# Kernel tuning notes

Measured on AMD Instinct MI355X. Metric: run time of the kernel, lower is better.

## Reference

```python
import jax, jax.numpy as jnp
import numpy as np


def setup_inputs() -> dict:
    key = jax.random.key(0)
    k1, k2 = jax.random.split(key)
    pred = jax.random.normal(k1, (128, 1024), dtype=jnp.float32)
    y = jax.random.normal(k2, (128, 1024), dtype=jnp.float32)
    return {"pred": pred, "y": y}


def reference(pred, y):
    # Original: transpose to [N, C], then per-column soft Kendall tau.
    p = pred.T  # [N, C]
    l = y.T     # [N, C]
    n = p.shape[0]
    # Pairwise outer differences, batched across all C columns at once: [N, N, C]
    diff = p[:, None, :] - p[None, :, :]
    sgn = jnp.sign(l[:, None, :] - l[None, :, :])
    tmp = jnp.tanh(diff * sgn)
    # Diagonal entries are tanh(0) = 0, so subtracting the eye-masked diagonal
    # (as in the original) is a no-op; just sum everything.
    per_col = jnp.sum(tmp, axis=(0, 1)) / (n * (n - 1))  # [C]
    return 1.0 - per_col.mean()
```

## Files before the change

### kernel.cpp

```cpp
#include <hip/hip_runtime.h>


typedef float v2f __attribute__((ext_vector_type(2)));

#define TAU_N 1024
#define TAU_C 128
#define TILE  256
#define NTILE (TAU_N / TILE)
#define NTP   (NTILE * (NTILE + 1) / 2)
#define PBLK  256
#define THR   1024
#define JOBS  ((TAU_C * NTP) / PBLK)
#define IT    4
#define JSL   16
#define JT    (TILE / JSL)

__device__ __constant__ int c_TI[NTP] = {0,1,1,2,2,2,3,3,3,3};
__device__ __constant__ int c_TJ[NTP] = {0,0,1,0,1,2,0,1,2,3};

__global__ __launch_bounds__(THR) void tau_tri_kernel(
        const float* __restrict__ pred, const float* __restrict__ y,
        float* __restrict__ out, float* __restrict__ acc_ws,
        unsigned* __restrict__ cnt_ws) {
    __shared__ __align__(16) float2 col[TAU_N];
    __shared__ float wsum[THR / 64];

    const int bx   = blockIdx.x;
    const int tid  = threadIdx.x;
    const int lane = tid & 63;
    const int wv   = tid >> 6;

    const int c = bx >> 1;
    const float* p = pred + c * TAU_N;
    const float* l = y    + c * TAU_N;

    col[tid] = make_float2(tanhf(p[tid]), l[tid]);
    __syncthreads();

    const float4* col4 = (const float4*)col;
    const v2f one2 = {1.f, 1.f};
    float acc_tot = 0.f;

#pragma unroll
    for (int q = 0; q < JOBS; ++q) {
        const int job = (bx & 1) * JOBS + q;
        const int ti  = c_TI[job];
        const int tj  = c_TJ[job];

        float mt[IT], ml[IT];
#pragma unroll
        for (int k = 0; k < IT; ++k) {
            float2 v = col[ti * TILE + lane * IT + k];
            mt[k] = v.x; ml[k] = v.y;
        }

        const int jb = (tj * TILE + wv * JT) >> 1;
        v2f acc[IT] = {{0.f,0.f},{0.f,0.f},{0.f,0.f},{0.f,0.f}};
#pragma unroll
        for (int jj = 0; jj < JT / 2; ++jj) {
            float4 qv = col4[jb + jj];
            v2f t2 = {qv.x, qv.z};
            v2f l2 = {qv.y, qv.w};
#pragma unroll
            for (int k = 0; k < IT; ++k) {
                v2f mt2 = {mt[k], mt[k]};
                v2f n2  = mt2 - t2;
                v2f d2  = __builtin_elementwise_fma(-mt2, t2, one2);
                v2f r2  = {__builtin_amdgcn_rcpf(d2.x),
                           __builtin_amdgcn_rcpf(d2.y)};
                v2f v2  = n2 * r2;
                v2f ld2 = (v2f){ml[k], ml[k]} - l2;
                unsigned sx = __float_as_uint(ld2.x) & 0x80000000u;
                unsigned sy = __float_as_uint(ld2.y) & 0x80000000u;
                acc[k] += (v2f){__uint_as_float(__float_as_uint(v2.x) ^ sx),
                                __uint_as_float(__float_as_uint(v2.y) ^ sy)};
            }
        }
        float a = (acc[0].x + acc[0].y) + (acc[1].x + acc[1].y)
                + (acc[2].x + acc[2].y) + (acc[3].x + acc[3].y);
        acc_tot += (ti == tj) ? 0.5f * a : a;
    }

    for (int off = 32; off >= 1; off >>= 1)
        acc_tot += __shfl_down(acc_tot, off, 64);
    if (lane == 0) wsum[wv] = acc_tot;
    __syncthreads();
    if (tid == 0) {
        float t = 0.f;
#pragma unroll
        for (int w = 0; w < THR / 64; ++w) t += wsum[w];
        atomicAdd(acc_ws, t);
        __threadfence();
        unsigned old = atomicAdd(cnt_ws, 1u);
        if (old == PBLK - 1) {
            __threadfence();
            float total = atomicAdd(acc_ws, 0.0f);
            const float scale = 2.0f / ((float)TAU_N * (float)(TAU_N - 1) * (float)TAU_C);
            out[0] = 1.0f - total * scale;
        }
    }
}

extern "C" void kernel_launch(void* const* d_in, const int* in_sizes, int n_in,
                              void* d_out, int out_size, void* d_ws, size_t ws_size,
                              hipStream_t stream) {
    const float* pred = (const float*)d_in[0];
    const float* y    = (const float*)d_in[1];
    float* out        = (float*)d_out;
    float* acc_ws     = (float*)d_ws;
    unsigned* cnt_ws  = (unsigned*)d_ws + 1;

    hipMemsetAsync(d_ws, 0, 2 * sizeof(unsigned), stream);
    tau_tri_kernel<<<PBLK, THR, 0, stream>>>(pred, y, out, acc_ws, cnt_ws);
}
```

Measured before the change: 77.10 us.

## Sort each column by label so pairwise sign terms become implicit

Each block now bitonic-sorts its column's (label, tanh(pred)) pairs in shared memory by label. After sorting, the sign of the label difference is fixed by index order, so the per-pair sign extraction and XOR go away. Only the lower-triangular pairs are accumulated, using smaller 128-wide tiles and 4 blocks per column. This trades a 55-stage shared-memory sort with many barriers per block for cheaper inner-loop arithmetic. Ties in labels are handled differently from sign(0)=0, which is negligible for continuous random inputs.

```diff
diff --git a/kernel.cpp b/kernel.cpp
--- a/kernel.cpp
+++ b/kernel.cpp
@@ -5,85 +5,111 @@
 
 #define TAU_N 1024
 #define TAU_C 128
-#define TILE  256
+#define TILE  128
 #define NTILE (TAU_N / TILE)
 #define NTP   (NTILE * (NTILE + 1) / 2)
-#define PBLK  256
+#define BPC   4
+#define JOBS  (NTP / BPC)
+#define PBLK  (TAU_C * BPC)
 #define THR   1024
-#define JOBS  ((TAU_C * NTP) / PBLK)
-#define IT    4
-#define JSL   16
-#define JT    (TILE / JSL)
 
-__device__ __constant__ int c_TI[NTP] = {0,1,1,2,2,2,3,3,3,3};
-__device__ __constant__ int c_TJ[NTP] = {0,0,1,0,1,2,0,1,2,3};
+__device__ __constant__ unsigned char c_TI[NTP] = {
+    0,1,1,2,2,2,3,3,3,3,4,4,4,4,4,5,5,5,5,5,5,
+    6,6,6,6,6,6,6,7,7,7,7,7,7,7,7};
+__device__ __constant__ unsigned char c_TJ[NTP] = {
+    0,0,1,0,1,2,0,1,2,3,0,1,2,3,4,0,1,2,3,4,5,
+    0,1,2,3,4,5,6,0,1,2,3,4,5,6,7};
 
-__global__ __launch_bounds__(THR) void tau_tri_kernel(
+__global__ __launch_bounds__(THR, 8) void tau_sorted_kernel(
         const float* __restrict__ pred, const float* __restrict__ y,
         float* __restrict__ out, float* __restrict__ acc_ws,
         unsigned* __restrict__ cnt_ws) {
-    __shared__ __align__(16) float2 col[TAU_N];
+    __shared__ __align__(16) float2 kv[TAU_N];
     __shared__ float wsum[THR / 64];
+    float* ts = (float*)kv;
 
-    const int bx   = blockIdx.x;
-    const int tid  = threadIdx.x;
-    const int lane = tid & 63;
-    const int wv   = tid >> 6;
+    const int bx  = blockIdx.x;
+    const int tid = threadIdx.x;
+    const int c   = bx >> 2;
+    const int jb0 = (bx & (BPC - 1)) * JOBS;
 
-    const int c = bx >> 1;
     const float* p = pred + c * TAU_N;
     const float* l = y    + c * TAU_N;
 
-    col[tid] = make_float2(tanhf(p[tid]), l[tid]);
+    kv[tid] = make_float2(l[tid], tanhf(p[tid]));
     __syncthreads();
 
-    const float4* col4 = (const float4*)col;
+    for (int k = 2; k <= TAU_N; k <<= 1) {
+        for (int j = k >> 1; j > 0; j >>= 1) {
+            const int ixj = tid ^ j;
+            if (ixj > tid) {
+                float2 a  = kv[tid];
+                float2 b2 = kv[ixj];
+                const bool up = ((tid & k) == 0);
+                if ((a.x > b2.x) == up) { kv[tid] = b2; kv[ixj] = a; }
+            }
+            __syncthreads();
+        }
+    }
+
+    const float tv = kv[tid].y;
+    __syncthreads();
+    ts[tid] = tv;
+    __syncthreads();
+
+    const float4* ts4 = (const float4*)ts;
+    const int ig = tid >> 5;
+    const int js = tid & 31;
     const v2f one2 = {1.f, 1.f};
-    float acc_tot = 0.f;
 
-#pragma unroll
+    v2f accA = {0.f, 0.f}, accB = {0.f, 0.f};
+    float acc_s = 0.f;
+
     for (int q = 0; q < JOBS; ++q) {
-        const int job = (bx & 1) * JOBS + q;
+        const int job = jb0 + q;
         const int ti  = c_TI[job];
         const int tj  = c_TJ[job];
-
-        float mt[IT], ml[IT];
+        const float4 mt4 = ts4[ti * (TILE / 4) + ig];
+        const float4 tq  = ts4[tj * (TILE / 4) + js];
+        if (ti != tj) {
+            const v2f t01 = {tq.x, tq.y};
+            const v2f t23 = {tq.z, tq.w};
+            const float mts[4] = {mt4.x, mt4.y, mt4.z, mt4.w};
 #pragma unroll
-        for (int k = 0; k < IT; ++k) {
-            float2 v = col[ti * TILE + lane * IT + k];
-            mt[k] = v.x; ml[k] = v.y;
-        }
-
-        const int jb = (tj * TILE + wv * JT) >> 1;
-        v2f acc[IT] = {{0.f,0.f},{0.f,0.f},{0.f,0.f},{0.f,0.f}};
+            for (int a = 0; a < 4; ++a) {
+                const v2f m2 = {mts[a], mts[a]};
+                v2f n01 = m2 - t01;
+                v2f n23 = m2 - t23;
+                v2f d01 = __builtin_elementwise_fma(-m2, t01, one2);
+                v2f d23 = __builtin_elementwise_fma(-m2, t23, one2);
+                v2f r01 = {__builtin_amdgcn_rcpf(d01.x),
+                           __builtin_amdgcn_rcpf(d01.y)};
+                v2f r23 = {__builtin_amdgcn_rcpf(d23.x),
+                           __builtin_amdgcn_rcpf(d23.y)};
+                accA = __builtin_elementwise_fma(n01, r01, accA);
+                accB = __builtin_elementwise_fma(n23, r23, accB);
+            }
+        } else {
+            const int gib = ig * 4, gjb = js * 4;
+            const float mts[4] = {mt4.x, mt4.y, mt4.z, mt4.w};
+            const float tjs[4] = {tq.x, tq.y, tq.z, tq.w};
 #pragma unroll
-        for (int jj = 0; jj < JT / 2; ++jj) {
-            float4 qv = col4[jb + jj];
-            v2f t2 = {qv.x, qv.z};
-            v2f l2 = {qv.y, qv.w};
+            for (int a = 0; a < 4; ++a) {
 #pragma unroll
-            for (int k = 0; k < IT; ++k) {
-                v2f mt2 = {mt[k], mt[k]};
-                v2f n2  = mt2 - t2;
-                v2f d2  = __builtin_elementwise_fma(-mt2, t2, one2);
-                v2f r2  = {__builtin_amdgcn_rcpf(d2.x),
-                           __builtin_amdgcn_rcpf(d2.y)};
-                v2f v2  = n2 * r2;
-                v2f ld2 = (v2f){ml[k], ml[k]} - l2;
-                unsigned sx = __float_as_uint(ld2.x) & 0x80000000u;
-                unsigned sy = __float_as_uint(ld2.y) & 0x80000000u;
-                acc[k] += (v2f){__uint_as_float(__float_as_uint(v2.x) ^ sx),
-                                __uint_as_float(__float_as_uint(v2.y) ^ sy)};
+                for (int b = 0; b < 4; ++b) {
+                    float n = mts[a] - tjs[b];
+                    float d = __builtin_fmaf(-mts[a], tjs[b], 1.f);
+                    float v = n * __builtin_amdgcn_rcpf(d);
+                    acc_s += (gib + a > gjb + b) ? v : 0.f;
+                }
             }
         }
-        float a = (acc[0].x + acc[0].y) + (acc[1].x + acc[1].y)
-                + (acc[2].x + acc[2].y) + (acc[3].x + acc[3].y);
-        acc_tot += (ti == tj) ? 0.5f * a : a;
     }
+    float acc = (accA.x + accA.y) + (accB.x + accB.y) + acc_s;
 
     for (int off = 32; off >= 1; off >>= 1)
-        acc_tot += __shfl_down(acc_tot, off, 64);
-    if (lane == 0) wsum[wv] = acc_tot;
+        acc += __shfl_down(acc, off, 64);
+    if ((tid & 63) == 0) wsum[tid >> 6] = acc;
     __syncthreads();
     if (tid == 0) {
         float t = 0.f;
@@ -111,5 +137,5 @@
     unsigned* cnt_ws  = (unsigned*)d_ws + 1;
 
     hipMemsetAsync(d_ws, 0, 2 * sizeof(unsigned), stream);
-    tau_tri_kernel<<<PBLK, THR, 0, stream>>>(pred, y, out, acc_ws, cnt_ws);
+    tau_sorted_kernel<<<PBLK, THR, 0, stream>>>(pred, y, out, acc_ws, cnt_ws);
 }
```

After: 91.40 us. +18.6%, slower.

## Use 128-wide tiles with 6 blocks per column and split tanh/label arrays

Applied to the files above, without the earlier changes.

Shrinks tiles to 128, giving 36 triangular tile pairs per column split across 6 blocks of 512 threads each (768 blocks in total instead of 256). Each thread now computes a fixed 8x4 micro-tile loaded with vector LDS reads from separate tanh and label arrays, replacing the old per-wave j-slice loop. The aims are better occupancy and load balance across CUs and cheaper shared-memory access. The cost is more blocks recomputing tanh for each column, more contention on the global atomics, and less work per thread to hide latency.

```diff
diff --git a/kernel.cpp b/kernel.cpp
--- a/kernel.cpp
+++ b/kernel.cpp
@@ -5,85 +5,104 @@
 
 #define TAU_N 1024
 #define TAU_C 128
-#define TILE  256
+#define TILE  128
 #define NTILE (TAU_N / TILE)
 #define NTP   (NTILE * (NTILE + 1) / 2)
-#define PBLK  256
-#define THR   1024
-#define JOBS  ((TAU_C * NTP) / PBLK)
-#define IT    4
-#define JSL   16
-#define JT    (TILE / JSL)
+#define BPC   6
+#define JOBS  (NTP / BPC)
+#define PBLK  (TAU_C * BPC)
+#define THR   512
+#define IT    8
 
-__device__ __constant__ int c_TI[NTP] = {0,1,1,2,2,2,3,3,3,3};
-__device__ __constant__ int c_TJ[NTP] = {0,0,1,0,1,2,0,1,2,3};
+__device__ __constant__ unsigned char c_TI[NTP] = {
+    0,1,1,2,2,2,3,3,3,3,4,4,4,4,4,5,5,5,5,5,5,
+    6,6,6,6,6,6,6,7,7,7,7,7,7,7,7};
+__device__ __constant__ unsigned char c_TJ[NTP] = {
+    0,0,1,0,1,2,0,1,2,3,0,1,2,3,4,0,1,2,3,4,5,
+    0,1,2,3,4,5,6,0,1,2,3,4,5,6,7};
 
-__global__ __launch_bounds__(THR) void tau_tri_kernel(
+__device__ __forceinline__ v2f tau_group(v2f m2, v2f mly, v2f t2, v2f l2, v2f acc) {
+    const v2f one2 = {1.f, 1.f};
+    v2f n  = m2 - t2;
+    v2f d  = __builtin_elementwise_fma(-m2, t2, one2);
+    v2f r  = {__builtin_amdgcn_rcpf(d.x), __builtin_amdgcn_rcpf(d.y)};
+    v2f v  = n * r;
+    v2f ld = mly - l2;
+    v2f sv = {__uint_as_float(__float_as_uint(v.x) ^
+                              (__float_as_uint(ld.x) & 0x80000000u)),
+              __uint_as_float(__float_as_uint(v.y) ^
+                              (__float_as_uint(ld.y) & 0x80000000u))};
+    return acc + sv;
+}
+
+__global__ __launch_bounds__(THR, 6) void tau_tri_kernel(
         const float* __restrict__ pred, const float* __restrict__ y,
         float* __restrict__ out, float* __restrict__ acc_ws,
         unsigned* __restrict__ cnt_ws) {
-    __shared__ __align__(16) float2 col[TAU_N];
+    __shared__ __align__(16) float ts[TAU_N];
+    __shared__ __align__(16) float ys[TAU_N];
     __shared__ float wsum[THR / 64];
 
-    const int bx   = blockIdx.x;
-    const int tid  = threadIdx.x;
-    const int lane = tid & 63;
-    const int wv   = tid >> 6;
+    const int bx  = blockIdx.x;
+    const int tid = threadIdx.x;
+    const int c   = bx / BPC;
+    const int jb0 = (bx % BPC) * JOBS;
 
-    const int c = bx >> 1;
     const float* p = pred + c * TAU_N;
     const float* l = y    + c * TAU_N;
 
-    col[tid] = make_float2(tanhf(p[tid]), l[tid]);
+    ts[tid]       = tanhf(p[tid]);
+    ts[tid + THR] = tanhf(p[tid + THR]);
+    ys[tid]       = l[tid];
+    ys[tid + THR] = l[tid + THR];
     __syncthreads();
 
-    const float4* col4 = (const float4*)col;
-    const v2f one2 = {1.f, 1.f};
+    const float4* t4 = (const float4*)ts;
+    const float4* y4 = (const float4*)ys;
+    const int ig = tid >> 5;
+    const int js = tid & 31;
+
     float acc_tot = 0.f;
 
 #pragma unroll
     for (int q = 0; q < JOBS; ++q) {
-        const int job = (bx & 1) * JOBS + q;
+        const int job = jb0 + q;
         const int ti  = c_TI[job];
         const int tj  = c_TJ[job];
 
-        float mt[IT], ml[IT];
+        const int ib4 = (ti * TILE + ig * IT) >> 2;
+        const float4 ta = t4[ib4], tb = t4[ib4 + 1];
+        const float4 la = y4[ib4], lb = y4[ib4 + 1];
+        const float mt[IT] = {ta.x, ta.y, ta.z, ta.w, tb.x, tb.y, tb.z, tb.w};
+        const float ml[IT] = {la.x, la.y, la.z, la.w, lb.x, lb.y, lb.z, lb.w};
+
+        const int jb4 = (tj * TILE + js * 4) >> 2;
+        const float4 tj4 = t4[jb4];
+        const float4 yj4 = y4[jb4];
+        const v2f tA = {tj4.x, tj4.y}, tB = {tj4.z, tj4.w};
+        const v2f lA = {yj4.x, yj4.y}, lB = {yj4.z, yj4.w};
+
+        v2f a0 = {0.f,0.f}, a1 = {0.f,0.f}, a2 = {0.f,0.f}, a3 = {0.f,0.f};
 #pragma unroll
-        for (int k = 0; k < IT; ++k) {
-            float2 v = col[ti * TILE + lane * IT + k];
-            mt[k] = v.x; ml[k] = v.y;
-        }
-
-        const int jb = (tj * TILE + wv * JT) >> 1;
-        v2f acc[IT] = {{0.f,0.f},{0.f,0.f},{0.f,0.f},{0.f,0.f}};
-#pragma unroll
-        for (int jj = 0; jj < JT / 2; ++jj) {
-            float4 qv = col4[jb + jj];
-            v2f t2 = {qv.x, qv.z};
-            v2f l2 = {qv.y, qv.w};
-#pragma unroll
-            for (int k = 0; k < IT; ++k) {
-                v2f mt2 = {mt[k], mt[k]};
-                v2f n2  = mt2 - t2;
-                v2f d2  = __builtin_elementwise_fma(-mt2, t2, one2);
-                v2f r2  = {__builtin_amdgcn_rcpf(d2.x),
-                           __builtin_amdgcn_rcpf(d2.y)};
-                v2f v2  = n2 * r2;
-                v2f ld2 = (v2f){ml[k], ml[k]} - l2;
-                unsigned sx = __float_as_uint(ld2.x) & 0x80000000u;
-                unsigned sy = __float_as_uint(ld2.y) & 0x80000000u;
-                acc[k] += (v2f){__uint_as_float(__float_as_uint(v2.x) ^ sx),
-                                __uint_as_float(__float_as_uint(v2.y) ^ sy)};
+        for (int a = 0; a < IT; ++a) {
+            const v2f m2  = {mt[a], mt[a]};
+            const v2f mly = {ml[a], ml[a]};
+            if (a & 1) {
+                a1 = tau_group(m2, mly, tA, lA, a1);
+                a3 = tau_group(m2, mly, tB, lB, a3);
+            } else {
+                a0 = tau_group(m2, mly, tA, lA, a0);
+                a2 = tau_group(m2, mly, tB, lB, a2);
             }
         }
-        float a = (acc[0].x + acc[0].y) + (acc[1].x + acc[1].y)
-                + (acc[2].x + acc[2].y) + (acc[3].x + acc[3].y);
-        acc_tot += (ti == tj) ? 0.5f * a : a;
+        const v2f asum = (a0 + a1) + (a2 + a3);
+        const float s = asum.x + asum.y;
+        acc_tot += (ti == tj) ? 0.5f * s : s;
     }
 
     for (int off = 32; off >= 1; off >>= 1)
         acc_tot += __shfl_down(acc_tot, off, 64);
-    if (lane == 0) wsum[wv] = acc_tot;
+    if ((tid & 63) == 0) wsum[tid >> 6] = acc_tot;
     __syncthreads();
     if (tid == 0) {
         float t = 0.f;
```

Result: slower. 80.56 us (+4.5%).
